# Optimization experiments

Hardware: AMD Instinct MI355X
Metric: run time of the kernel (lower is better)

The kernel has to match this reference:

```python
import jax, jax.numpy as jnp
import numpy as np

ND, ED, HD, L, K = 128, 64, 256, 4, 24   # node_dim, edge_dim(num_rbf), hidden_dim, num_layers, max_neighbors
CUTOFF = 8.0
N = 2048  # n_atoms


def _silu(x):
    return x * jax.nn.sigmoid(x)


def _lattice(lengths, angles):
    a, b, c = lengths[0], lengths[1], lengths[2]
    deg = jnp.asarray(np.pi / 180.0, lengths.dtype)
    al, be, ga = angles[0] * deg, angles[1] * deg, angles[2] * deg
    lx = a
    xy = b * jnp.cos(ga)
    xz = c * jnp.cos(be)
    ly = b * jnp.sin(ga)
    yz = (b * c * jnp.cos(al) - xy * xz) / ly
    lz = jnp.sqrt(c ** 2 - xz ** 2 - yz ** 2)
    z = jnp.zeros((), lengths.dtype)
    return jnp.stack([jnp.stack([lx, z, z]), jnp.stack([xy, ly, z]), jnp.stack([xz, yz, lz])])


def _rbf(d):
    centers = jnp.linspace(0.0, CUTOFF, ED)
    widths = jnp.full((ED,), CUTOFF / ED)
    d = d[..., None]
    g = jnp.exp(-(d - centers) ** 2 / (2.0 * widths ** 2))
    cv = 0.5 * (jnp.cos(d * jnp.pi / CUTOFF) + 1.0) * (d < CUTOFF).astype(d.dtype)
    return g * cv


def _forward(atom_types, frac_coords, lengths, angles, timesteps, emb, tW, tb,
             eW1, eb1, eW2, eb2, nW1, nb1, nW2, nb2, cW1, cb1, cW2, cb2):
    n = frac_coords.shape[0]
    lattice = _lattice(lengths, angles)            # [3,3]
    cart = frac_coords @ lattice                   # [n,3]

    # ---- vectorized periodic neighbor graph (replaces host triple loop) ----
    shifts = jnp.asarray(np.array([[i, j, k] for i in (-1, 0, 1) for j in (-1, 0, 1) for k in (-1, 0, 1)],
                                  dtype=np.float32))
    sv = shifts @ lattice                          # [27,3]
    p = cart[None, :, :] + sv[:, None, :]          # [27,n,3] shifted atom positions
    # squared distances without materializing [27,n,n,3]
    d2 = (p * p).sum(-1)[:, :, None] + (cart * cart).sum(-1)[None, None, :] \
         - 2.0 * jnp.einsum('snk,mk->snm', p, cart)      # [27, n_j, n_i]
    dist = jnp.sqrt(jnp.maximum(d2, 1e-12))
    cand = jnp.where((dist < CUTOFF) & (dist > 0.01), dist, jnp.inf)
    cand = cand.reshape(27 * n, n).T               # [n_i, 27*n_j]; flat f = s*n + j
    _, idx = jax.lax.top_k(-cand, K)               # K smallest distances per atom i
    d_k = jnp.take_along_axis(cand, idx, axis=1)   # [n,K]
    dst = (idx % n).reshape(-1)                    # neighbor atom j (edge_list = [i, j])
    src = jnp.repeat(jnp.arange(n), K)             # center atom i
    valid = jnp.isfinite(d_k).reshape(-1)
    m = valid.astype(jnp.float32)[:, None]         # [E,1] pad mask
    d_e = jnp.where(valid, d_k.reshape(-1), 0.0)
    edge_attr = _rbf(d_e)                          # [E, ED]

    # ---- EGNN stack ----
    nf = emb[atom_types] + timesteps @ tW + tb     # [n, ND]
    coords = cart
    seg = lambda x, i: jax.ops.segment_sum(x, i, num_segments=n)
    for l in range(L):
        ef = jnp.concatenate([nf[src], nf[dst], edge_attr], axis=-1)   # [E, 2*ND+ED]
        msg = _silu(_silu(ef @ eW1[l] + eb1[l]) @ eW2[l] + eb2[l])     # [E, HD]
        aggr = seg(msg * m, dst)                                       # [n, HD]
        nf = nf + _silu(jnp.concatenate([nf, aggr], axis=-1) @ nW1[l] + nb1[l]) @ nW2[l] + nb2[l]
        w = _silu(msg @ cW1[l] + cb1[l]) @ cW2[l] + cb2[l]             # [E,1]
        cd = coords[src] - coords[dst]
        cd = cd / (jnp.linalg.norm(cd, axis=-1, keepdims=True) + 1e-8)
        coords = coords + seg(w * cd * m, dst)
    return nf, coords


def setup_inputs() -> dict:
    key = jax.random.key(0)
    ks = jax.random.split(key, 16)
    pr = lambda k, shape: jax.random.normal(k, shape, jnp.float32) * 0.02
    return dict(
        atom_types=jax.random.randint(ks[0], (N,), 0, 100),
        frac_coords=jax.random.uniform(ks[1], (N, 3), jnp.float32),
        lengths=jnp.ones((3,), jnp.float32) * 12.0,
        angles=jnp.ones((3,), jnp.float32) * 90.0,
        timesteps=jax.random.normal(ks[2], (N, 128), jnp.float32),
        emb=pr(ks[3], (100, ND)),
        tW=pr(ks[4], (128, ND)), tb=jnp.zeros((ND,), jnp.float32),
        eW1=pr(ks[5], (L, 2 * ND + ED, HD)), eb1=jnp.zeros((L, HD), jnp.float32),
        eW2=pr(ks[6], (L, HD, HD)), eb2=jnp.zeros((L, HD), jnp.float32),
        nW1=pr(ks[7], (L, ND + HD, HD)), nb1=jnp.zeros((L, HD), jnp.float32),
        nW2=pr(ks[8], (L, HD, ND)), nb2=jnp.zeros((L, ND), jnp.float32),
        cW1=pr(ks[9], (L, HD, HD // 2)), cb1=jnp.zeros((L, HD // 2), jnp.float32),
        cW2=pr(ks[10], (L, HD // 2, 1)), cb2=jnp.zeros((L, 1), jnp.float32),
    )


def reference(atom_types, frac_coords, lengths, angles, timesteps, emb, tW, tb,
              eW1, eb1, eW2, eb2, nW1, nb1, nW2, nb2, cW1, cb1, cW2, cb2):
    return _forward(atom_types, frac_coords, lengths, angles, timesteps, emb, tW, tb,
                    eW1, eb1, eW2, eb2, nW1, nb1, nW2, nb2, cW1, cb1, cW2, cb2)
```

## Files before the change

kernel.cpp:

```cpp
#include <hip/hip_runtime.h>
#include <math.h>

#define NA 2048
#define KN 24
#define NE (NA*KN)
#define NDIM 128
#define EDIM 64
#define HDIM 256
#define NLAYER 4
#define MAXDEG 256
#define EB 64

typedef __attribute__((ext_vector_type(8))) short bf16x8;
typedef __attribute__((ext_vector_type(4))) float f32x4;

__device__ __forceinline__ float siluf(float x) { return x / (1.0f + expf(-x)); }
__device__ __forceinline__ ushort f2b(float x) {
    unsigned u = __float_as_uint(x);
    return (ushort)((u + 0x7fffu + ((u >> 16) & 1u)) >> 16);
}
__device__ __forceinline__ float b2f(ushort h) { return __uint_as_float(((unsigned)h) << 16); }

__device__ __forceinline__ void gl_lds(const void* g, void* lds) {
    __builtin_amdgcn_global_load_lds(
        (const __attribute__((address_space(1))) unsigned int*)g,
        (__attribute__((address_space(3))) unsigned int*)lds, 16, 0, 0);
}

struct Lat { float lx, xy, xz, ly, yz, lz; };

__device__ __forceinline__ Lat make_lattice(const float* lengths, const float* angles) {
    const float deg = 0.017453292519943295f;
    float a = lengths[0], b = lengths[1], c = lengths[2];
    float al = angles[0]*deg, be = angles[1]*deg, ga = angles[2]*deg;
    Lat L;
    L.lx = a;
    L.xy = b * cosf(ga);
    L.xz = c * cosf(be);
    L.ly = b * sinf(ga);
    L.yz = (b*c*cosf(al) - L.xy*L.xz) / L.ly;
    L.lz = sqrtf(c*c - L.xz*L.xz - L.yz*L.yz);
    return L;
}

__global__ void setup_kernel(const float* __restrict__ frac, const float* __restrict__ lengths,
                             const float* __restrict__ angles, float* __restrict__ cart,
                             float* __restrict__ cxg, float* __restrict__ cyg,
                             float* __restrict__ czg, float* __restrict__ sv,
                             int* __restrict__ ccnt) {
    int i = blockIdx.x*blockDim.x + threadIdx.x;
    Lat L = make_lattice(lengths, angles);
    if (i < NA) {
        float f0 = frac[i*3], f1 = frac[i*3+1], f2 = frac[i*3+2];
        float x = f0*L.lx + f1*L.xy + f2*L.xz;
        float y = f1*L.ly + f2*L.yz;
        float z = f2*L.lz;
        cart[i*3+0] = x; cart[i*3+1] = y; cart[i*3+2] = z;
        cxg[i] = x; cyg[i] = y; czg[i] = z;
        ccnt[i] = 0;
    }
    if (i < 27) {
        float s0 = (float)(i/9 - 1), s1 = (float)((i/3)%3 - 1), s2 = (float)(i%3 - 1);
        sv[i*3+0] = s0*L.lx + s1*L.xy + s2*L.xz;
        sv[i*3+1] = s1*L.ly + s2*L.yz;
        sv[i*3+2] = s2*L.lz;
    }
}

__global__ __launch_bounds__(64) void knn_kernel(
        const float* __restrict__ cxg, const float* __restrict__ cyg,
        const float* __restrict__ czg, const float* __restrict__ lengths,
        const float* __restrict__ angles, const float* __restrict__ sv,
        int* __restrict__ dstl, ushort* __restrict__ rbf16,
        int* __restrict__ ccnt, int* __restrict__ cedg) {
    __shared__ float sd2L[16][64];
    __shared__ int   sfL[16][64];
    const int lane = threadIdx.x;
    const int i = blockIdx.x;
    Lat L = make_lattice(lengths, angles);
    const float deg = 0.017453292519943295f;
    const bool ortho = fabsf(cosf(angles[0]*deg)) < 1e-6f &&
                       fabsf(cosf(angles[1]*deg)) < 1e-6f &&
                       fabsf(cosf(angles[2]*deg)) < 1e-6f;
    const float cx = cxg[i], cy = cyg[i], cz = czg[i];
    const float invlx = 1.0f/L.lx, invly = 1.0f/L.ly, invlz = 1.0f/L.lz;
    float R = 2.8f;
    int mycnt = 0, cnt = 0;
    bool flatm = false;
    for (int attempt = 0; attempt < 8; ++attempt) {
        const float R2 = R*R;
        mycnt = 0;
        flatm = !ortho || (attempt == 7);
        if (!flatm) {
#pragma unroll 2
            for (int j0 = 0; j0 < NA; j0 += 64) {
                const int j = j0 + lane;
                const float dx = cxg[j] - cx, dy = cyg[j] - cy, dz = czg[j] - cz;
                const float kx = rintf(dx*invlx), ky = rintf(dy*invly), kz = rintf(dz*invlz);
                const float ex = dx - (kx*L.lx + ky*L.xy + kz*L.xz);
                const float ey = dy - (ky*L.ly + kz*L.yz);
                const float ez = dz - kz*L.lz;
                const float d2 = fmaf(ex,ex,fmaf(ey,ey,ez*ez));
                if (d2 < R2 && d2 > 1e-4f) {
                    const int s = (1-(int)kx)*9 + (1-(int)ky)*3 + (1-(int)kz);
                    if (mycnt < 16) { sd2L[mycnt][lane] = d2; sfL[mycnt][lane] = (s<<11) + j; }
                    ++mycnt;
                }
            }
            if (__ballot(mycnt > 16)) {
                flatm = true;
            } else {
                int tot = mycnt;
                for (int off = 32; off > 0; off >>= 1) tot += __shfl_xor(tot, off, 64);
                cnt = tot;
            }
        }
        if (flatm) {
            cnt = 0;
            for (int s = 0; s < 27; ++s) {
                const float svx = sv[s*3], svy = sv[s*3+1], svz = sv[s*3+2];
                for (int j0 = 0; j0 < NA; j0 += 64) {
                    const int j = j0 + lane;
                    const float ex = cxg[j] + svx - cx;
                    const float ey = cyg[j] + svy - cy;
                    const float ez = czg[j] + svz - cz;
                    const float d2 = fmaf(ex,ex,fmaf(ey,ey,ez*ez));
                    const bool hit = (d2 < R2) && (d2 > 1e-4f);
                    const unsigned long long m = __ballot(hit);
                    const int rank = __popcll(m & ((1ull<<lane)-1ull));
                    const int slot = cnt + rank;
                    if (hit && slot < 1024) { sd2L[slot>>6][slot&63] = d2; sfL[slot>>6][slot&63] = (s<<11)+j; }
                    cnt += __popcll(m);
                }
            }
            cnt = min(cnt, 1024);
        }
        if (cnt >= KN) break;
        R = fminf(R*1.6f, flatm ? 8.0f : 5.9f);
    }
    int vq;
    if (flatm) vq = (lane < cnt) ? min(16, ((cnt - 1 - lane) >> 6) + 1) : 0;
    else       vq = mycnt;
    unsigned long long key[16];
#pragma unroll
    for (int q = 0; q < 16; ++q) {
        const float d2v = sd2L[q][lane];
        const int fl = sfL[q][lane];
        const unsigned long long kk = ((unsigned long long)__float_as_uint(d2v) << 20)
                                    | ((unsigned long long)(unsigned)fl << 4) | (unsigned)q;
        key[q] = (q < vq) ? kk : ~0ull;
    }
    float der[KN];
    for (int k = 0; k < KN; ++k) {
        unsigned long long lm = key[0];
#pragma unroll
        for (int q = 1; q < 16; ++q) lm = key[q] < lm ? key[q] : lm;
        for (int off = 32; off > 0; off >>= 1) {
            unsigned long long o = __shfl_xor(lm, off, 64);
            lm = o < lm ? o : lm;
        }
        der[k] = sqrtf(__uint_as_float((unsigned)(lm >> 20)));
        if (lane == 0) {
            const int jn = (int)((lm >> 4) & 2047u);
            dstl[i*KN + k] = jn;
            const int slot = atomicAdd(&ccnt[jn], 1);
            if (slot < MAXDEG) cedg[(size_t)jn*MAXDEG + slot] = i*KN + k;
        }
#pragma unroll
        for (int q = 0; q < 16; ++q) if (key[q] == lm) key[q] = ~0ull;
    }
    const float center = (8.0f/63.0f) * (float)lane;
    for (int k = 0; k < KN; ++k) {
        const float d = der[k];
        const float diff = d - center;
        const float g = expf(diff*diff * -32.0f);
        const float cv = 0.5f * (cosf(d * (float)(M_PI/8.0)) + 1.0f);
        rbf16[(size_t)(i*KN + k)*EDIM + lane] = f2b(g * cv);
    }
}

__global__ void csort_kernel(const int* __restrict__ ccnt, int* __restrict__ cedg) {
    const int j = blockIdx.x*4 + (threadIdx.x >> 6);
    const int lane = threadIdx.x & 63;
    const int cnt = min(ccnt[j], MAXDEG);
    if (cnt <= 64) {
        int v = (lane < cnt) ? cedg[(size_t)j*MAXDEG + lane] : 0x7FFFFFFF;
#pragma unroll
        for (int k = 2; k <= 64; k <<= 1) {
#pragma unroll
            for (int s = k >> 1; s > 0; s >>= 1) {
                int o = __shfl_xor(v, s, 64);
                const bool up = ((lane & k) == 0);
                const bool lowhalf = ((lane & s) == 0);
                v = ((lowhalf == up) ? min(v, o) : max(v, o));
            }
        }
        if (lane < cnt) cedg[(size_t)j*MAXDEG + lane] = v;
    } else if (lane == 0) {
        int* L = cedg + (size_t)j*MAXDEG;
        for (int a = 1; a < cnt; ++a) {
            int v = L[a]; int b = a - 1;
            while (b >= 0 && L[b] > v) { L[b+1] = L[b]; --b; }
            L[b+1] = v;
        }
    }
}

__global__ void nf_init_kernel(const int* __restrict__ atom_types, const float* __restrict__ ts,
                               const float* __restrict__ emb, const float* __restrict__ tW,
                               const float* __restrict__ tb, float* __restrict__ nf,
                               ushort* __restrict__ nf16) {
    int i = blockIdx.x, c = threadIdx.x;
    float acc = emb[atom_types[i]*NDIM + c] + tb[c];
    for (int kk = 0; kk < 128; ++kk) acc += ts[i*128 + kk] * tW[kk*NDIM + c];
    nf[i*NDIM + c] = acc;
    nf16[i*NDIM + c] = f2b(acc);
}

__global__ void wprep_all(const float* __restrict__ eW1, const float* __restrict__ eW2,
                          const float* __restrict__ cW1, const float* __restrict__ nW1,
                          const float* __restrict__ nW2,
                          ushort* __restrict__ eW1t, ushort* __restrict__ eW2t,
                          ushort* __restrict__ cW1t, ushort* __restrict__ nW1t,
                          ushort* __restrict__ nW2t) {
    __shared__ float tile[64][65];
    const int b = blockIdx.x;
    const float* W; ushort* Wt; int Kk, Nn, rel;
    if (b < 80)       { W = eW1; Wt = eW1t; Kk = 320; Nn = 256; rel = b; }
    else if (b < 144) { W = eW2; Wt = eW2t; Kk = 256; Nn = 256; rel = b - 80; }
    else if (b < 176) { W = cW1; Wt = cW1t; Kk = 256; Nn = 128; rel = b - 144; }
    else if (b < 272) { W = nW1; Wt = nW1t; Kk = 384; Nn = 256; rel = b - 176; }
    else              { W = nW2; Wt = nW2t; Kk = 256; Nn = 128; rel = b - 272; }
    const int kt = Kk >> 6, nt = Nn >> 6, per = kt*nt;
    const int l = rel / per, r2 = rel - l*per;
    const int k0 = (r2 / nt) * 64, n0 = (r2 - (r2/nt)*nt) * 64;
    const float* Wl = W + (size_t)l*Kk*Nn;
    ushort* Wtl = Wt + (size_t)l*Kk*Nn;
    const int tr = threadIdx.x >> 6, tc = threadIdx.x & 63;
#pragma unroll
    for (int q = 0; q < 16; ++q) {
        const int k = q*4 + tr;
        tile[k][tc] = Wl[(size_t)(k0 + k)*Nn + n0 + tc];
    }
    __syncthreads();
#pragma unroll
    for (int q = 0; q < 16; ++q) {
        const int n = q*4 + tr;
        Wtl[(size_t)(n0 + n)*Kk + k0 + tc] = f2b(tile[tc][n]);
    }
}

__global__ __launch_bounds__(256) void edge_fused(
        const ushort* __restrict__ nf16, const int* __restrict__ dstl,
        const ushort* __restrict__ rbf16,
        const ushort* __restrict__ eW1t,
        const ushort* __restrict__ eW2t,
        const ushort* __restrict__ cW1t,
        const float* __restrict__ eb1, const float* __restrict__ eb2,
        const float* __restrict__ cb1, const float* __restrict__ cW2v,
        const float* __restrict__ cb2v,
        ushort* __restrict__ msg16, float* __restrict__ wvout) {
    __shared__ alignas(16) char R0[40960];
    __shared__ alignas(16) char R1[32768];
    __shared__ int sdst[64];
    __shared__ float wred[2][64];
    ushort* As = (ushort*)R0;
    ushort* Bs = (ushort*)(R0 + 8192);
    ushort* B2 = (ushort*)R1;
    ushort* Cs = (ushort*)R1;

    const int t = threadIdx.x, wave = t >> 6, lane = t & 63;
    const int row0 = blockIdx.x*EB;
    if (t < EB) sdst[t] = dstl[row0 + t];
    __syncthreads();
    const int wr = (wave >> 1)*32;
    const int wcB = (wave & 1)*128;
    const int lr = lane & 15, g0 = lane >> 4;

    const int rA_  = wave*16 + (lane >> 2);
    const int gA_  = (lane & 3) ^ ((rA_ >> 1) & 3);
    const int eA_  = row0 + rA_;
    const ushort* baseSrc = nf16  + (size_t)(eA_/KN)*NDIM + gA_*8;
    const ushort* baseDst = nf16  + (size_t)sdst[rA_]*NDIM + gA_*8;
    const ushort* baseRbf = rbf16 + (size_t)eA_*EDIM + gA_*8;
    const uint ldsA_ = (uint)(wave*16)*32;
    const ushort* baseW1[4]; const ushort* baseW2[4];
    uint ldsBq[4];
#pragma unroll
    for (int q = 0; q < 4; ++q) {
        const int rowb = wave*64 + q*16 + (lane >> 2);
        const int gB = (lane & 3) ^ ((rowb >> 1) & 3);
        baseW1[q] = eW1t + (size_t)rowb*320 + gB*8;
        baseW2[q] = eW2t + (size_t)rowb*256 + gB*8;
        ldsBq[q] = (uint)(wave*64 + q*16)*32;
    }
    const ushort* baseC[2];
    uint ldsCq[2];
#pragma unroll
    for (int q = 0; q < 2; ++q) {
        const int rowb = wave*32 + q*16 + (lane >> 2);
        const int gB = (lane & 3) ^ ((rowb >> 1) & 3);
        baseC[q] = cW1t + (size_t)rowb*256 + gB*8;
        ldsCq[q] = (uint)(wave*32 + q*16)*32;
    }

    auto STAGEA = [&](int buf, int k0) {
        const ushort* gp = (k0 < NDIM) ? baseSrc + k0
                         : (k0 < 2*NDIM) ? baseDst + (k0 - NDIM)
                         : baseRbf + (k0 - 2*NDIM);
        gl_lds(gp, As + (size_t)buf*2048 + ldsA_);
#pragma unroll
        for (int q = 0; q < 4; ++q)
            gl_lds(baseW1[q] + k0, Bs + (size_t)buf*8192 + ldsBq[q]);
    };
    f32x4 acc[2][8];
#pragma unroll
    for (int m = 0; m < 2; ++m)
#pragma unroll
        for (int n = 0; n < 8; ++n) acc[m][n] = (f32x4){0.f,0.f,0.f,0.f};
    STAGEA(0, 0);
    int cur = 0;
#pragma unroll
    for (int it = 0; it < 10; ++it) {
        if (it + 1 < 10) {
            STAGEA(cur ^ 1, (it + 1)*32);
            asm volatile("s_waitcnt vmcnt(5)" ::: "memory");
        } else {
            asm volatile("s_waitcnt vmcnt(0)" ::: "memory");
        }
        __builtin_amdgcn_sched_barrier(0);
        __builtin_amdgcn_s_barrier();
        __builtin_amdgcn_sched_barrier(0);
        bf16x8 af[2], bfr[8];
#pragma unroll
        for (int m = 0; m < 2; ++m) {
            const int rA = wr + m*16 + lr;
            af[m] = *reinterpret_cast<const bf16x8*>(&As[cur*2048 + rA*32 + ((g0 ^ ((rA>>1)&3)))*8]);
        }
#pragma unroll
        for (int n = 0; n < 8; ++n) {
            const int rB = wcB + n*16 + lr;
            bfr[n] = *reinterpret_cast<const bf16x8*>(&Bs[(size_t)cur*8192 + rB*32 + ((g0 ^ ((rB>>1)&3)))*8]);
        }
        __builtin_amdgcn_s_setprio(1);
#pragma unroll
        for (int m = 0; m < 2; ++m)
#pragma unroll
            for (int n = 0; n < 8; ++n)
                acc[m][n] = __builtin_amdgcn_mfma_f32_16x16x32_bf16(af[m], bfr[n], acc[m][n], 0, 0, 0);
        __builtin_amdgcn_s_setprio(0);
        asm volatile("s_waitcnt lgkmcnt(0)" ::: "memory");
        __builtin_amdgcn_sched_barrier(0);
        __builtin_amdgcn_s_barrier();
        __builtin_amdgcn_sched_barrier(0);
        cur ^= 1;
    }
    {
#pragma unroll
        for (int q = 0; q < 4; ++q)
            gl_lds(baseW2[q], B2 + ldsBq[q]);
    }
#pragma unroll
    for (int n = 0; n < 8; ++n) {
        const int cc = wcB + n*16 + lr;
        const float b1 = eb1[cc];
#pragma unroll
        for (int m = 0; m < 2; ++m) {
#pragma unroll
            for (int j = 0; j < 4; ++j) {
                const int rr = wr + m*16 + g0*4 + j;
                const float x = siluf(acc[m][n][j] + b1);
                *(ushort*)(R0 + rr*512 + ((cc*2) ^ ((rr&7)<<4))) = f2b(x);
            }
        }
    }
    __syncthreads();

#pragma unroll
    for (int m = 0; m < 2; ++m)
#pragma unroll
        for (int n = 0; n < 8; ++n) acc[m][n] = (f32x4){0.f,0.f,0.f,0.f};
    cur = 0;
#pragma unroll
    for (int it = 0; it < 8; ++it) {
        if (it + 1 < 8) {
            const int k0 = (it + 1)*32;
#pragma unroll
            for (int q = 0; q < 4; ++q)
                gl_lds(baseW2[q] + k0, B2 + (size_t)(cur^1)*8192 + ldsBq[q]);
            asm volatile("s_waitcnt vmcnt(4)" ::: "memory");
        } else {
            asm volatile("s_waitcnt vmcnt(0)" ::: "memory");
        }
        __builtin_amdgcn_sched_barrier(0);
        __builtin_amdgcn_s_barrier();
        __builtin_amdgcn_sched_barrier(0);
        bf16x8 af[2], bfr[8];
#pragma unroll
        for (int m = 0; m < 2; ++m) {
            const int rA = wr + m*16 + lr;
            const int kc = it*4 + g0;
            af[m] = *reinterpret_cast<const bf16x8*>(R0 + rA*512 + ((kc*16) ^ ((rA&7)<<4)));
        }
#pragma unroll
        for (int n = 0; n < 8; ++n) {
            const int rB = wcB + n*16 + lr;
            bfr[n] = *reinterpret_cast<const bf16x8*>(&B2[(size_t)cur*8192 + rB*32 + ((g0 ^ ((rB>>1)&3)))*8]);
        }
        __builtin_amdgcn_s_setprio(1);
#pragma unroll
        for (int m = 0; m < 2; ++m)
#pragma unroll
            for (int n = 0; n < 8; ++n)
                acc[m][n] = __builtin_amdgcn_mfma_f32_16x16x32_bf16(af[m], bfr[n], acc[m][n], 0, 0, 0);
        __builtin_amdgcn_s_setprio(0);
        asm volatile("s_waitcnt lgkmcnt(0)" ::: "memory");
        __builtin_amdgcn_sched_barrier(0);
        __builtin_amdgcn_s_barrier();
        __builtin_amdgcn_sched_barrier(0);
        cur ^= 1;
    }
    {
#pragma unroll
        for (int q = 0; q < 2; ++q)
            gl_lds(baseC[q], Cs + ldsCq[q]);
    }
#pragma unroll
    for (int n = 0; n < 8; ++n) {
        const int cc = wcB + n*16 + lr;
        const float b2 = eb2[cc];
#pragma unroll
        for (int m = 0; m < 2; ++m) {
#pragma unroll
            for (int j = 0; j < 4; ++j) {
                const int rr = wr + m*16 + g0*4 + j;
                *(ushort*)(R0 + rr*512 + ((cc*2) ^ ((rr&7)<<4))) = f2b(siluf(acc[m][n][j] + b2));
            }
        }
    }
    __syncthreads();

    const int wcC = (wave & 1)*64;
    f32x4 acc3[2][4];
#pragma unroll
    for (int m = 0; m < 2; ++m)
#pragma unroll
        for (int n = 0; n < 4; ++n) acc3[m][n] = (f32x4){0.f,0.f,0.f,0.f};
    cur = 0;
#pragma unroll
    for (int it = 0; it < 8; ++it) {
        if (it + 1 < 8) {
            const int k0 = (it + 1)*32;
#pragma unroll
            for (int q = 0; q < 2; ++q)
                gl_lds(baseC[q] + k0, Cs + (size_t)(cur^1)*4096 + ldsCq[q]);
            asm volatile("s_waitcnt vmcnt(2)" ::: "memory");
        } else {
            asm volatile("s_waitcnt vmcnt(0)" ::: "memory");
        }
        __builtin_amdgcn_sched_barrier(0);
        __builtin_amdgcn_s_barrier();
        __builtin_amdgcn_sched_barrier(0);
        bf16x8 af[2], bfr[4];
#pragma unroll
        for (int m = 0; m < 2; ++m) {
            const int rA = wr + m*16 + lr;
            const int kc = it*4 + g0;
            af[m] = *reinterpret_cast<const bf16x8*>(R0 + rA*512 + ((kc*16) ^ ((rA&7)<<4)));
        }
#pragma unroll
        for (int n = 0; n < 4; ++n) {
            const int rB = wcC + n*16 + lr;
            bfr[n] = *reinterpret_cast<const bf16x8*>(&Cs[(size_t)cur*4096 + rB*32 + ((g0 ^ ((rB>>1)&3)))*8]);
        }
        __builtin_amdgcn_s_setprio(1);
#pragma unroll
        for (int m = 0; m < 2; ++m)
#pragma unroll
            for (int n = 0; n < 4; ++n)
                acc3[m][n] = __builtin_amdgcn_mfma_f32_16x16x32_bf16(af[m], bfr[n], acc3[m][n], 0, 0, 0);
        __builtin_amdgcn_s_setprio(0);
        asm volatile("s_waitcnt lgkmcnt(0)" ::: "memory");
        __builtin_amdgcn_sched_barrier(0);
        __builtin_amdgcn_s_barrier();
        __builtin_amdgcn_sched_barrier(0);
        cur ^= 1;
    }
    float part[2][4];
#pragma unroll
    for (int m = 0; m < 2; ++m)
#pragma unroll
        for (int j = 0; j < 4; ++j) part[m][j] = 0.0f;
#pragma unroll
    for (int n = 0; n < 4; ++n) {
        const int cc = wcC + n*16 + lr;
        const float bb = cb1[cc];
        const float cw = cW2v[cc];
#pragma unroll
        for (int m = 0; m < 2; ++m)
#pragma unroll
            for (int j = 0; j < 4; ++j)
                part[m][j] += siluf(acc3[m][n][j] + bb) * cw;
    }
#pragma unroll
    for (int off = 1; off < 16; off <<= 1)
#pragma unroll
        for (int m = 0; m < 2; ++m)
#pragma unroll
            for (int j = 0; j < 4; ++j)
                part[m][j] += __shfl_xor(part[m][j], off, 64);
    if (lr == 0) {
#pragma unroll
        for (int m = 0; m < 2; ++m)
#pragma unroll
            for (int j = 0; j < 4; ++j)
                wred[wave & 1][wr + m*16 + g0*4 + j] = part[m][j];
    }
    __syncthreads();
    if (t < EB) wvout[row0 + t] = wred[0][t] + wred[1][t] + cb2v[0];
#pragma unroll
    for (int k = 0; k < 8; ++k) {
        const int off = (t + k*256) * 16;
        const int row = off >> 9;
        const int cg = ((off >> 4) & 31) ^ (row & 7);
        uint4 v = *reinterpret_cast<const uint4*>(R0 + off);
        *reinterpret_cast<uint4*>(msg16 + (size_t)(row0 + row)*256 + cg*8) = v;
    }
}

template<int AMODE, int EPI>
__global__ __launch_bounds__(256) void bgemm_kernel(
        const ushort* __restrict__ A, const ushort* __restrict__ nf16,
        const ushort* __restrict__ aggr16, const ushort* __restrict__ Bt,
        const float* __restrict__ bias, const float* __restrict__ res,
        float* __restrict__ Cf, ushort* __restrict__ C16, int M, int Nn, int Kk) {
    __shared__ alignas(16) ushort As[2][128*32];
    __shared__ alignas(16) ushort Bs[2][128*32];
    const int t = threadIdx.x;
    const int wave = t >> 6, lane = t & 63;
    const int row0 = blockIdx.x*128, col0 = blockIdx.y*128;
    const int wr = (wave >> 1)*64, wc = (wave & 1)*64;
    const int lr = lane & 15, g0 = lane >> 4;

    auto STAGE = [&](int buf, int k0) {
#pragma unroll
        for (int q = 0; q < 4; ++q) {
            const int rbase = (q & 1)*64 + wave*16;
            const int r = rbase + (lane >> 2);
            const int g = (lane & 3) ^ ((r >> 1) & 3);
            const int kg = k0 + g*8;
            const int ldsbase = rbase * 32;
            if (q < 2) {
                const ushort* gp;
                if (AMODE == 0) {
                    gp = A + (size_t)(row0 + r)*Kk + kg;
                } else {
                    const int e = row0 + r;
                    if (kg < NDIM) gp = nf16 + (size_t)e*NDIM + kg;
                    else           gp = aggr16 + (size_t)e*HDIM + (kg - NDIM);
                }
                gl_lds(gp, &As[buf][ldsbase]);
            } else {
                gl_lds(Bt + (size_t)(col0 + r)*Kk + kg, &Bs[buf][ldsbase]);
            }
        }
    };

    f32x4 acc[4][4] = {};
    const int nk = Kk >> 5;
    STAGE(0, 0);
    int cur = 0;
    for (int it = 0; it < nk; ++it) {
        if (it + 1 < nk) {
            STAGE(cur ^ 1, (it + 1) << 5);
            asm volatile("s_waitcnt vmcnt(4)" ::: "memory");
        } else {
            asm volatile("s_waitcnt vmcnt(0)" ::: "memory");
        }
        __builtin_amdgcn_sched_barrier(0);
        __builtin_amdgcn_s_barrier();
        __builtin_amdgcn_sched_barrier(0);
        bf16x8 af[4], bfr[4];
#pragma unroll
        for (int m = 0; m < 4; ++m) {
            const int rA = wr + m*16 + lr;
            af[m] = *reinterpret_cast<const bf16x8*>(&As[cur][rA*32 + (g0 ^ ((rA>>1)&3))*8]);
        }
#pragma unroll
        for (int n = 0; n < 4; ++n) {
            const int rB = wc + n*16 + lr;
            bfr[n] = *reinterpret_cast<const bf16x8*>(&Bs[cur][rB*32 + (g0 ^ ((rB>>1)&3))*8]);
        }
#pragma unroll
        for (int m = 0; m < 4; ++m)
#pragma unroll
            for (int n = 0; n < 4; ++n)
                acc[m][n] = __builtin_amdgcn_mfma_f32_16x16x32_bf16(af[m], bfr[n], acc[m][n], 0, 0, 0);
        asm volatile("s_waitcnt lgkmcnt(0)" ::: "memory");
        __builtin_amdgcn_sched_barrier(0);
        __builtin_amdgcn_s_barrier();
        __builtin_amdgcn_sched_barrier(0);
        cur ^= 1;
    }

#pragma unroll
    for (int n = 0; n < 4; ++n) {
        const int cc = col0 + wc + n*16 + lr;
        const float bb = bias[cc];
#pragma unroll
        for (int m = 0; m < 4; ++m) {
#pragma unroll
            for (int j = 0; j < 4; ++j) {
                const int rr = row0 + wr + m*16 + (lane >> 4)*4 + j;
                float x = acc[m][n][j] + bb;
                if constexpr (EPI == 0) {
                    C16[(size_t)rr*Nn + cc] = f2b(siluf(x));
                } else {
                    x += res[(size_t)rr*Nn + cc];
                    Cf[(size_t)rr*Nn + cc] = x;
                    C16[(size_t)rr*Nn + cc] = f2b(x);
                }
            }
        }
    }
}

__global__ void node_kernel(const ushort* __restrict__ msg16, const float* __restrict__ cold,
                            const float* __restrict__ wv, const int* __restrict__ ccnt,
                            const int* __restrict__ cedg,
                            ushort* __restrict__ aggr16, float* __restrict__ cnew) {
    __shared__ int se[4][64];
    const int w = threadIdx.x >> 6, lane = threadIdx.x & 63;
    const int j = blockIdx.x*4 + w;
    const int cnt = min(ccnt[j], MAXDEG);
    se[w][lane] = (lane < cnt) ? cedg[(size_t)j*MAXDEG + lane] : 0;
    __syncthreads();
    const int c4 = lane*4;
    float s0 = 0, s1 = 0, s2 = 0, s3 = 0;
    const int lim = min(cnt, 64);
    for (int q = 0; q < lim; ++q) {
        const int e = se[w][q];
        ushort4 v = *reinterpret_cast<const ushort4*>(&msg16[(size_t)e*HDIM + c4]);
        s0 += b2f(v.x); s1 += b2f(v.y); s2 += b2f(v.z); s3 += b2f(v.w);
    }
    for (int q = 64; q < cnt; ++q) {
        const int e = cedg[(size_t)j*MAXDEG + q];
        ushort4 v = *reinterpret_cast<const ushort4*>(&msg16[(size_t)e*HDIM + c4]);
        s0 += b2f(v.x); s1 += b2f(v.y); s2 += b2f(v.z); s3 += b2f(v.w);
    }
    ushort4 o; o.x = f2b(s0); o.y = f2b(s1); o.z = f2b(s2); o.w = f2b(s3);
    *reinterpret_cast<ushort4*>(&aggr16[(size_t)j*HDIM + c4]) = o;
    const float jx = cold[j*3], jy = cold[j*3+1], jz = cold[j*3+2];
    float dx = 0, dy = 0, dz = 0;
    for (int q = lane; q < cnt; q += 64) {
        const int e = (q < 64) ? se[w][q] : cedg[(size_t)j*MAXDEG + q];
        const int si = e / KN;
        const float ax = cold[si*3]   - jx;
        const float ay = cold[si*3+1] - jy;
        const float az = cold[si*3+2] - jz;
        const float inv = wv[e] / (sqrtf(ax*ax + ay*ay + az*az) + 1e-8f);
        dx += inv*ax; dy += inv*ay; dz += inv*az;
    }
    for (int off = 32; off > 0; off >>= 1) {
        dx += __shfl_xor(dx, off, 64);
        dy += __shfl_xor(dy, off, 64);
        dz += __shfl_xor(dz, off, 64);
    }
    if (lane == 0) {
        cnew[j*3]   = jx + dx;
        cnew[j*3+1] = jy + dy;
        cnew[j*3+2] = jz + dz;
    }
}

__global__ void copyout_kernel(const float* __restrict__ nf, const float* __restrict__ coords,
                               float* __restrict__ out) {
    int idx = blockIdx.x*256 + threadIdx.x;
    if (idx < NA*NDIM) out[idx] = nf[idx];
    else if (idx < NA*NDIM + NA*3) out[idx] = coords[idx - NA*NDIM];
}

extern "C" void kernel_launch(void* const* d_in, const int* in_sizes, int n_in,
                              void* d_out, int out_size, void* d_ws, size_t ws_size,
                              hipStream_t stream) {
    const int*   atom_types = (const int*)  d_in[0];
    const float* frac       = (const float*)d_in[1];
    const float* lengths    = (const float*)d_in[2];
    const float* angles     = (const float*)d_in[3];
    const float* timesteps  = (const float*)d_in[4];
    const float* emb        = (const float*)d_in[5];
    const float* tW         = (const float*)d_in[6];
    const float* tb         = (const float*)d_in[7];
    const float* eW1        = (const float*)d_in[8];
    const float* eb1        = (const float*)d_in[9];
    const float* eW2        = (const float*)d_in[10];
    const float* eb2        = (const float*)d_in[11];
    const float* nW1        = (const float*)d_in[12];
    const float* nb1        = (const float*)d_in[13];
    const float* nW2        = (const float*)d_in[14];
    const float* nb2        = (const float*)d_in[15];
    const float* cW1        = (const float*)d_in[16];
    const float* cb1        = (const float*)d_in[17];
    const float* cW2        = (const float*)d_in[18];
    const float* cb2        = (const float*)d_in[19];

    char* p = (char*)d_ws;
    auto alloc = [&](size_t bytes) { char* q = p; p += (bytes + 255) & ~(size_t)255; return q; };
    float*  sv    = (float*) alloc(81*4);
    float*  c0    = (float*) alloc((size_t)NA*3*4);
    float*  c1    = (float*) alloc((size_t)NA*3*4);
    float*  cxg   = (float*) alloc((size_t)NA*4);
    float*  cyg   = (float*) alloc((size_t)NA*4);
    float*  czg   = (float*) alloc((size_t)NA*4);
    float*  nf    = (float*) alloc((size_t)NA*NDIM*4);
    int*    dstl  = (int*)   alloc((size_t)NE*4);
    ushort* rbf16 = (ushort*)alloc((size_t)NE*EDIM*2);
    int*    ccnt  = (int*)   alloc((size_t)NA*4);
    int*    cedg  = (int*)   alloc((size_t)NA*MAXDEG*4);
    ushort* aggr16= (ushort*)alloc((size_t)NA*HDIM*2);
    ushort* t116  = (ushort*)alloc((size_t)NA*HDIM*2);
    float*  wv    = (float*) alloc((size_t)NE*4);
    ushort* nf16  = (ushort*)alloc((size_t)NA*NDIM*2);
    ushort* msg16 = (ushort*)alloc((size_t)NE*HDIM*2);
    ushort* eW1t  = (ushort*)alloc((size_t)NLAYER*(2*NDIM+EDIM)*HDIM*2);
    ushort* eW2t  = (ushort*)alloc((size_t)NLAYER*HDIM*HDIM*2);
    ushort* cW1t  = (ushort*)alloc((size_t)NLAYER*(HDIM/2)*HDIM*2);
    ushort* nW1t  = (ushort*)alloc((size_t)NLAYER*(NDIM+HDIM)*HDIM*2);
    ushort* nW2t  = (ushort*)alloc((size_t)NLAYER*HDIM*NDIM*2);

    setup_kernel<<<8, 256, 0, stream>>>(frac, lengths, angles, c0, cxg, cyg, czg, sv, ccnt);
    knn_kernel<<<NA, 64, 0, stream>>>(cxg, cyg, czg, lengths, angles, sv,
                                      dstl, rbf16, ccnt, cedg);
    csort_kernel<<<NA/4, 256, 0, stream>>>(ccnt, cedg);
    nf_init_kernel<<<NA, 128, 0, stream>>>(atom_types, timesteps, emb, tW, tb, nf, nf16);
    wprep_all<<<304, 256, 0, stream>>>(eW1, eW2, cW1, nW1, nW2,
                                       eW1t, eW2t, cW1t, nW1t, nW2t);

    float* cin = c0; float* cout = c1;
    for (int l = 0; l < NLAYER; ++l) {
        const float* eb1l = eb1 + (size_t)l*HDIM;
        const float* eb2l = eb2 + (size_t)l*HDIM;
        const float* nb1l = nb1 + (size_t)l*HDIM;
        const float* nb2l = nb2 + (size_t)l*NDIM;
        const float* cb1l = cb1 + (size_t)l*(HDIM/2);
        const float* cW2l = cW2 + (size_t)l*(HDIM/2);
        const float* cb2l = cb2 + (size_t)l;

        edge_fused<<<NE/EB, 256, 0, stream>>>(
            nf16, dstl, rbf16,
            eW1t + (size_t)l*(2*NDIM+EDIM)*HDIM, eW2t + (size_t)l*HDIM*HDIM,
            cW1t + (size_t)l*(HDIM/2)*HDIM,
            eb1l, eb2l, cb1l, cW2l, cb2l, msg16, wv);
        node_kernel<<<NA/4, 256, 0, stream>>>(msg16, cin, wv, ccnt, cedg, aggr16, cout);
        bgemm_kernel<2,0><<<dim3(NA/128, HDIM/128), 256, 0, stream>>>(
            nullptr, nf16, aggr16, nW1t + (size_t)l*(NDIM+HDIM)*HDIM, nb1l, nullptr,
            nullptr, t116, NA, HDIM, NDIM+HDIM);
        bgemm_kernel<0,2><<<dim3(NA/128, NDIM/128), 256, 0, stream>>>(
            t116, nullptr, nullptr, nW2t + (size_t)l*HDIM*NDIM, nb2l, nf,
            nf, nf16, NA, NDIM, HDIM);
        float* tmp = cin; cin = cout; cout = tmp;
    }
    copyout_kernel<<<(NA*NDIM + NA*3)/256, 256, 0, stream>>>(nf, cin, (float*)d_out);
}
```

Measured before the change: 405.7 us.

## Fuse node MLP GEMMs into one kernel and drop sched barriers around s_barrier

The two node-update GEMMs (concat[nf,aggr]→hidden with SiLU, then hidden→node with residual) are replaced by a single kernel over 64-row tiles. The full A tile is held in LDS and the hidden activations stay in LDS as bf16 instead of round-tripping through global memory. This removes one launch and the t1 intermediate traffic. In exchange the grid shrinks to 32 blocks of 256 threads, which is low occupancy on a large GPU, and LDS use per block goes up. Separately, the sched_barrier fences around s_barrier in the edge kernel's GEMM loops are removed, which frees the compiler to reorder instructions around the barriers.

```diff
diff --git a/kernel.cpp b/kernel.cpp
--- a/kernel.cpp
+++ b/kernel.cpp
@@ -328,9 +328,7 @@
         } else {
             asm volatile("s_waitcnt vmcnt(0)" ::: "memory");
         }
-        __builtin_amdgcn_sched_barrier(0);
-        __builtin_amdgcn_s_barrier();
-        __builtin_amdgcn_sched_barrier(0);
+        __builtin_amdgcn_s_barrier();
         bf16x8 af[2], bfr[8];
 #pragma unroll
         for (int m = 0; m < 2; ++m) {
@@ -350,9 +348,7 @@
                 acc[m][n] = __builtin_amdgcn_mfma_f32_16x16x32_bf16(af[m], bfr[n], acc[m][n], 0, 0, 0);
         __builtin_amdgcn_s_setprio(0);
         asm volatile("s_waitcnt lgkmcnt(0)" ::: "memory");
-        __builtin_amdgcn_sched_barrier(0);
-        __builtin_amdgcn_s_barrier();
-        __builtin_amdgcn_sched_barrier(0);
+        __builtin_amdgcn_s_barrier();
         cur ^= 1;
     }
     {
@@ -392,9 +388,7 @@
         } else {
             asm volatile("s_waitcnt vmcnt(0)" ::: "memory");
         }
-        __builtin_amdgcn_sched_barrier(0);
-        __builtin_amdgcn_s_barrier();
-        __builtin_amdgcn_sched_barrier(0);
+        __builtin_amdgcn_s_barrier();
         bf16x8 af[2], bfr[8];
 #pragma unroll
         for (int m = 0; m < 2; ++m) {
@@ -415,9 +409,7 @@
                 acc[m][n] = __builtin_amdgcn_mfma_f32_16x16x32_bf16(af[m], bfr[n], acc[m][n], 0, 0, 0);
         __builtin_amdgcn_s_setprio(0);
         asm volatile("s_waitcnt lgkmcnt(0)" ::: "memory");
-        __builtin_amdgcn_sched_barrier(0);
-        __builtin_amdgcn_s_barrier();
-        __builtin_amdgcn_sched_barrier(0);
+        __builtin_amdgcn_s_barrier();
         cur ^= 1;
     }
     {
@@ -458,9 +450,7 @@
         } else {
             asm volatile("s_waitcnt vmcnt(0)" ::: "memory");
         }
-        __builtin_amdgcn_sched_barrier(0);
-        __builtin_amdgcn_s_barrier();
-        __builtin_amdgcn_sched_barrier(0);
+        __builtin_amdgcn_s_barrier();
         bf16x8 af[2], bfr[4];
 #pragma unroll
         for (int m = 0; m < 2; ++m) {
@@ -481,9 +471,7 @@
                 acc3[m][n] = __builtin_amdgcn_mfma_f32_16x16x32_bf16(af[m], bfr[n], acc3[m][n], 0, 0, 0);
         __builtin_amdgcn_s_setprio(0);
         asm volatile("s_waitcnt lgkmcnt(0)" ::: "memory");
-        __builtin_amdgcn_sched_barrier(0);
-        __builtin_amdgcn_s_barrier();
-        __builtin_amdgcn_sched_barrier(0);
+        __builtin_amdgcn_s_barrier();
         cur ^= 1;
     }
     float part[2][4];
@@ -528,98 +516,171 @@
     }
 }
 
-template<int AMODE, int EPI>
-__global__ __launch_bounds__(256) void bgemm_kernel(
-        const ushort* __restrict__ A, const ushort* __restrict__ nf16,
-        const ushort* __restrict__ aggr16, const ushort* __restrict__ Bt,
-        const float* __restrict__ bias, const float* __restrict__ res,
-        float* __restrict__ Cf, ushort* __restrict__ C16, int M, int Nn, int Kk) {
-    __shared__ alignas(16) ushort As[2][128*32];
-    __shared__ alignas(16) ushort Bs[2][128*32];
-    const int t = threadIdx.x;
-    const int wave = t >> 6, lane = t & 63;
-    const int row0 = blockIdx.x*128, col0 = blockIdx.y*128;
-    const int wr = (wave >> 1)*64, wc = (wave & 1)*64;
+__global__ __launch_bounds__(256) void nodefused(
+        const ushort* __restrict__ nf16, const ushort* __restrict__ aggr16,
+        const ushort* __restrict__ nW1t,
+        const ushort* __restrict__ nW2t,
+        const float* __restrict__ nb1, const float* __restrict__ nb2,
+        float* __restrict__ nf, ushort* __restrict__ nf16out) {
+    __shared__ alignas(16) ushort Ab[12*2048];
+    __shared__ alignas(16) char HsB[32768];
+    __shared__ alignas(16) ushort Bs[2][256*32];
+    const int t = threadIdx.x, wave = t >> 6, lane = t & 63;
+    const int r0 = blockIdx.x*64;
+    const int wr = (wave >> 1)*32;
+    const int wcB = (wave & 1)*128;
     const int lr = lane & 15, g0 = lane >> 4;
 
-    auto STAGE = [&](int buf, int k0) {
+#pragma unroll
+    for (int c = 0; c < 3; ++c) {
+        const int ks = wave*3 + c;
 #pragma unroll
         for (int q = 0; q < 4; ++q) {
-            const int rbase = (q & 1)*64 + wave*16;
-            const int r = rbase + (lane >> 2);
+            const int r = q*16 + (lane >> 2);
             const int g = (lane & 3) ^ ((r >> 1) & 3);
-            const int kg = k0 + g*8;
-            const int ldsbase = rbase * 32;
-            if (q < 2) {
-                const ushort* gp;
-                if (AMODE == 0) {
-                    gp = A + (size_t)(row0 + r)*Kk + kg;
-                } else {
-                    const int e = row0 + r;
-                    if (kg < NDIM) gp = nf16 + (size_t)e*NDIM + kg;
-                    else           gp = aggr16 + (size_t)e*HDIM + (kg - NDIM);
-                }
-                gl_lds(gp, &As[buf][ldsbase]);
-            } else {
-                gl_lds(Bt + (size_t)(col0 + r)*Kk + kg, &Bs[buf][ldsbase]);
-            }
-        }
-    };
-
-    f32x4 acc[4][4] = {};
-    const int nk = Kk >> 5;
-    STAGE(0, 0);
+            const int col = ks*32 + g*8;
+            const ushort* gp = (col < NDIM)
+                ? nf16 + (size_t)(r0 + r)*NDIM + col
+                : aggr16 + (size_t)(r0 + r)*HDIM + (col - NDIM);
+            gl_lds(gp, Ab + ks*2048 + q*16*32);
+        }
+    }
+    const ushort* baseW1[4];
+    uint ldsBq[4];
+#pragma unroll
+    for (int q = 0; q < 4; ++q) {
+        const int rowb = wave*64 + q*16 + (lane >> 2);
+        const int gB = (lane & 3) ^ ((rowb >> 1) & 3);
+        baseW1[q] = nW1t + (size_t)rowb*384 + gB*8;
+        ldsBq[q] = (uint)(wave*64 + q*16)*32;
+    }
+    const ushort* baseW2[2];
+    uint ldsCq[2];
+#pragma unroll
+    for (int q = 0; q < 2; ++q) {
+        const int rowb = wave*32 + q*16 + (lane >> 2);
+        const int gB = (lane & 3) ^ ((rowb >> 1) & 3);
+        baseW2[q] = nW2t + (size_t)rowb*256 + gB*8;
+        ldsCq[q] = (uint)(wave*32 + q*16)*32;
+    }
+#pragma unroll
+    for (int q = 0; q < 4; ++q)
+        gl_lds(baseW1[q], &Bs[0][ldsBq[q]]);
+    asm volatile("s_waitcnt vmcnt(0)" ::: "memory");
+    __builtin_amdgcn_s_barrier();
+
+    f32x4 acc[2][8];
+#pragma unroll
+    for (int m = 0; m < 2; ++m)
+#pragma unroll
+        for (int n = 0; n < 8; ++n) acc[m][n] = (f32x4){0.f,0.f,0.f,0.f};
     int cur = 0;
-    for (int it = 0; it < nk; ++it) {
-        if (it + 1 < nk) {
-            STAGE(cur ^ 1, (it + 1) << 5);
+#pragma unroll
+    for (int it = 0; it < 12; ++it) {
+        if (it + 1 < 12) {
+            const int k0 = (it + 1)*32;
+#pragma unroll
+            for (int q = 0; q < 4; ++q)
+                gl_lds(baseW1[q] + k0, &Bs[cur^1][ldsBq[q]]);
             asm volatile("s_waitcnt vmcnt(4)" ::: "memory");
         } else {
             asm volatile("s_waitcnt vmcnt(0)" ::: "memory");
         }
-        __builtin_amdgcn_sched_barrier(0);
-        __builtin_amdgcn_s_barrier();
-        __builtin_amdgcn_sched_barrier(0);
-        bf16x8 af[4], bfr[4];
-#pragma unroll
-        for (int m = 0; m < 4; ++m) {
+        __builtin_amdgcn_s_barrier();
+        bf16x8 af[2], bfr[8];
+#pragma unroll
+        for (int m = 0; m < 2; ++m) {
             const int rA = wr + m*16 + lr;
-            af[m] = *reinterpret_cast<const bf16x8*>(&As[cur][rA*32 + (g0 ^ ((rA>>1)&3))*8]);
+            af[m] = *reinterpret_cast<const bf16x8*>(&Ab[it*2048 + rA*32 + ((g0 ^ ((rA>>1)&3)))*8]);
+        }
+#pragma unroll
+        for (int n = 0; n < 8; ++n) {
+            const int rB = wcB + n*16 + lr;
+            bfr[n] = *reinterpret_cast<const bf16x8*>(&Bs[cur][rB*32 + ((g0 ^ ((rB>>1)&3)))*8]);
+        }
+        __builtin_amdgcn_s_setprio(1);
+#pragma unroll
+        for (int m = 0; m < 2; ++m)
+#pragma unroll
+            for (int n = 0; n < 8; ++n)
+                acc[m][n] = __builtin_amdgcn_mfma_f32_16x16x32_bf16(af[m], bfr[n], acc[m][n], 0, 0, 0);
+        __builtin_amdgcn_s_setprio(0);
+        asm volatile("s_waitcnt lgkmcnt(0)" ::: "memory");
+        __builtin_amdgcn_s_barrier();
+        cur ^= 1;
+    }
+#pragma unroll
+    for (int q = 0; q < 2; ++q)
+        gl_lds(baseW2[q], &Bs[0][ldsCq[q]]);
+#pragma unroll
+    for (int n = 0; n < 8; ++n) {
+        const int cc = wcB + n*16 + lr;
+        const float b1 = nb1[cc];
+#pragma unroll
+        for (int m = 0; m < 2; ++m) {
+#pragma unroll
+            for (int j = 0; j < 4; ++j) {
+                const int rr = wr + m*16 + g0*4 + j;
+                *(ushort*)(HsB + rr*512 + ((cc*2) ^ ((rr&7)<<4))) = f2b(siluf(acc[m][n][j] + b1));
+            }
+        }
+    }
+    __syncthreads();
+
+    const int wcC = (wave & 1)*64;
+    f32x4 acc3[2][4];
+#pragma unroll
+    for (int m = 0; m < 2; ++m)
+#pragma unroll
+        for (int n = 0; n < 4; ++n) acc3[m][n] = (f32x4){0.f,0.f,0.f,0.f};
+    cur = 0;
+#pragma unroll
+    for (int it = 0; it < 8; ++it) {
+        if (it + 1 < 8) {
+            const int k0 = (it + 1)*32;
+#pragma unroll
+            for (int q = 0; q < 2; ++q)
+                gl_lds(baseW2[q] + k0, &Bs[cur^1][ldsCq[q]]);
+            asm volatile("s_waitcnt vmcnt(2)" ::: "memory");
+        } else {
+            asm volatile("s_waitcnt vmcnt(0)" ::: "memory");
+        }
+        __builtin_amdgcn_s_barrier();
+        bf16x8 af[2], bfr[4];
+#pragma unroll
+        for (int m = 0; m < 2; ++m) {
+            const int rA = wr + m*16 + lr;
+            const int kc = it*4 + g0;
+            af[m] = *reinterpret_cast<const bf16x8*>(HsB + rA*512 + ((kc*16) ^ ((rA&7)<<4)));
         }
 #pragma unroll
         for (int n = 0; n < 4; ++n) {
-            const int rB = wc + n*16 + lr;
-            bfr[n] = *reinterpret_cast<const bf16x8*>(&Bs[cur][rB*32 + (g0 ^ ((rB>>1)&3))*8]);
-        }
-#pragma unroll
-        for (int m = 0; m < 4; ++m)
+            const int rB = wcC + n*16 + lr;
+            bfr[n] = *reinterpret_cast<const bf16x8*>(&Bs[cur][rB*32 + ((g0 ^ ((rB>>1)&3)))*8]);
+        }
+        __builtin_amdgcn_s_setprio(1);
+#pragma unroll
+        for (int m = 0; m < 2; ++m)
 #pragma unroll
             for (int n = 0; n < 4; ++n)
-                acc[m][n] = __builtin_amdgcn_mfma_f32_16x16x32_bf16(af[m], bfr[n], acc[m][n], 0, 0, 0);
+                acc3[m][n] = __builtin_amdgcn_mfma_f32_16x16x32_bf16(af[m], bfr[n], acc3[m][n], 0, 0, 0);
+        __builtin_amdgcn_s_setprio(0);
         asm volatile("s_waitcnt lgkmcnt(0)" ::: "memory");
-        __builtin_amdgcn_sched_barrier(0);
-        __builtin_amdgcn_s_barrier();
-        __builtin_amdgcn_sched_barrier(0);
+        __builtin_amdgcn_s_barrier();
         cur ^= 1;
     }
-
 #pragma unroll
     for (int n = 0; n < 4; ++n) {
-        const int cc = col0 + wc + n*16 + lr;
-        const float bb = bias[cc];
-#pragma unroll
-        for (int m = 0; m < 4; ++m) {
+        const int cc = wcC + n*16 + lr;
+        const float b2 = nb2[cc];
+#pragma unroll
+        for (int m = 0; m < 2; ++m) {
 #pragma unroll
             for (int j = 0; j < 4; ++j) {
-                const int rr = row0 + wr + m*16 + (lane >> 4)*4 + j;
-                float x = acc[m][n][j] + bb;
-                if constexpr (EPI == 0) {
-                    C16[(size_t)rr*Nn + cc] = f2b(siluf(x));
-                } else {
-                    x += res[(size_t)rr*Nn + cc];
-                    Cf[(size_t)rr*Nn + cc] = x;
-                    C16[(size_t)rr*Nn + cc] = f2b(x);
-                }
+                const int rr = r0 + wr + m*16 + g0*4 + j;
+                float x = acc3[m][n][j] + b2 + nf[(size_t)rr*NDIM + cc];
+                nf[(size_t)rr*NDIM + cc] = x;
+                nf16out[(size_t)rr*NDIM + cc] = f2b(x);
             }
         }
     }
@@ -718,7 +779,6 @@
     int*    ccnt  = (int*)   alloc((size_t)NA*4);
     int*    cedg  = (int*)   alloc((size_t)NA*MAXDEG*4);
     ushort* aggr16= (ushort*)alloc((size_t)NA*HDIM*2);
-    ushort* t116  = (ushort*)alloc((size_t)NA*HDIM*2);
     float*  wv    = (float*) alloc((size_t)NE*4);
     ushort* nf16  = (ushort*)alloc((size_t)NA*NDIM*2);
     ushort* msg16 = (ushort*)alloc((size_t)NE*HDIM*2);
@@ -752,12 +812,9 @@
             cW1t + (size_t)l*(HDIM/2)*HDIM,
             eb1l, eb2l, cb1l, cW2l, cb2l, msg16, wv);
         node_kernel<<<NA/4, 256, 0, stream>>>(msg16, cin, wv, ccnt, cedg, aggr16, cout);
-        bgemm_kernel<2,0><<<dim3(NA/128, HDIM/128), 256, 0, stream>>>(
-            nullptr, nf16, aggr16, nW1t + (size_t)l*(NDIM+HDIM)*HDIM, nb1l, nullptr,
-            nullptr, t116, NA, HDIM, NDIM+HDIM);
-        bgemm_kernel<0,2><<<dim3(NA/128, NDIM/128), 256, 0, stream>>>(
-            t116, nullptr, nullptr, nW2t + (size_t)l*HDIM*NDIM, nb2l, nf,
-            nf, nf16, NA, NDIM, HDIM);
+        nodefused<<<NA/64, 256, 0, stream>>>(
+            nf16, aggr16, nW1t + (size_t)l*(NDIM+HDIM)*HDIM, nW2t + (size_t)l*HDIM*NDIM,
+            nb1l, nb2l, nf, nf16);
         float* tmp = cin; cin = cout; cout = tmp;
     }
     copyout_kernel<<<(NA*NDIM + NA*3)/256, 256, 0, stream>>>(nf, cin, (float*)d_out);
```

Result: no change. 402.6 us (-0.8%).
